# Kernel optimization log

Hardware: AMD Instinct MI355X
Metric: run time of the kernel (lower is better)

## Reference

```python
import jax, jax.numpy as jnp
import numpy as np

# Geometry constants matching __init__ defaults
DG = 2        # deformable_groups
KS = 3        # kernel_size
K = KS * KS   # taps per kernel
DIL = 2       # dilation
PAD = 2       # padding = dilation
STRIDE = 1


def setup_inputs() -> dict:
    key = jax.random.key(0)
    k1, k2, k3, k4 = jax.random.split(key, 4)
    B, C, H, W = 4, 128, 96, 192
    Cout = 128
    x = jax.random.normal(k1, (B, C, H, W), dtype=jnp.float32)
    # offset/mask conv: grouped conv, groups=DG -> in-channels per group = C//DG
    off_out = DG * 3 * K  # 54 (36 offset + 18 mask)
    # small weights so learned offsets are O(1) pixels (realistic trained regime;
    # the original zero-init would make the gather trivial)
    w_offset = jax.random.normal(k2, (off_out, C // DG, KS, KS), dtype=jnp.float32) * 0.01
    b_offset = jax.random.normal(k3, (off_out,), dtype=jnp.float32) * 0.1
    stdv = 1.0 / np.sqrt(C * KS * KS)
    w_deform = jax.random.uniform(k4, (Cout, C, KS, KS), dtype=jnp.float32,
                                  minval=-stdv, maxval=stdv)
    return {"x": x, "w_offset": w_offset, "b_offset": b_offset, "w_deform": w_deform}


def _deform_conv2d(x, w_offset, b_offset, w_deform):
    B, C, H, W = x.shape
    Cout = w_deform.shape[0]
    Cg = C // DG
    # --- offset/mask conv (grouped, dilated) ---
    om = jax.lax.conv_general_dilated(
        x, w_offset, (STRIDE, STRIDE), [(PAD, PAD), (PAD, PAD)],
        rhs_dilation=(DIL, DIL), feature_group_count=DG,
        dimension_numbers=("NCHW", "OIHW", "NCHW"))
    om = om + b_offset[None, :, None, None]
    Ho, Wo = om.shape[2], om.shape[3]
    off_ch = DG * 2 * K
    offset = om[:, :off_ch]                       # [B, 36, Ho, Wo]
    mask = jax.nn.sigmoid(om[:, off_ch:]) * 2.0   # double_mask=True -> *2
    # torchvision layout: channel 2*(g*K+k) = dy, +1 = dx
    off = offset.reshape(B, DG, K, 2, Ho, Wo)
    m = mask.reshape(B, DG, K, Ho, Wo)
    # --- sampling coordinates ---
    ky = (jnp.arange(K) // KS).astype(x.dtype)
    kx = (jnp.arange(K) % KS).astype(x.dtype)
    base_y = (jnp.arange(Ho) * STRIDE - PAD).astype(x.dtype)
    base_x = (jnp.arange(Wo) * STRIDE - PAD).astype(x.dtype)
    py = base_y[None, None, None, :, None] + (ky * DIL)[None, None, :, None, None] + off[:, :, :, 0]
    px = base_x[None, None, None, None, :] + (kx * DIL)[None, None, :, None, None] + off[:, :, :, 1]
    y0 = jnp.floor(py)
    x0 = jnp.floor(px)
    ty = py - y0
    tx = px - x0
    xflat = x.reshape(B, DG, Cg, H * W)
    # gather[b,g,c,n] = xflat[b,g,c, idx[b,g,n]]
    gather = jax.vmap(jax.vmap(lambda xg, idx: jnp.take(xg, idx, axis=1)))
    val = jnp.zeros((B, DG, Cg, K, Ho, Wo), x.dtype)
    # accumulate bilinear corners one at a time to bound peak memory
    for dy, dx, wgt in ((0, 0, (1 - ty) * (1 - tx)), (0, 1, (1 - ty) * tx),
                        (1, 0, ty * (1 - tx)), (1, 1, ty * tx)):
        yy = y0 + dy
        xx = x0 + dx
        valid = (yy >= 0) & (yy < H) & (xx >= 0) & (xx < W)
        yc = jnp.clip(yy, 0, H - 1).astype(jnp.int32)
        xc = jnp.clip(xx, 0, W - 1).astype(jnp.int32)
        lin = (yc * W + xc).reshape(B, DG, K * Ho * Wo)
        g = gather(xflat, lin).reshape(B, DG, Cg, K, Ho, Wo)
        val = val + jnp.where(valid, wgt, 0.0)[:, :, None] * g
    val = val * m[:, :, None]  # modulation mask per deformable group / tap
    wr = w_deform.reshape(Cout, DG, Cg, K)
    return jnp.einsum("ogck,bgckhw->bohw", wr, val)


def reference(x, w_offset, b_offset, w_deform):
    return _deform_conv2d(x, w_offset, b_offset, w_deform)
```

## Files before the change

### kernel.cpp

```cpp
#include <hip/hip_runtime.h>
#include <hip/hip_fp16.h>
#include <math.h>

#define BB   4
#define C_   128
#define H_   96
#define W_   192
#define COUT 128
#define DG_  2
#define CG_  64
#define K_   9
#define HO   96
#define WO   192
#define HW   (H_ * W_)
#define OMCH 54
#define RDIM (C_ * K_)
#define NKS  (RDIM / 32)
#define CSTEP 2
#define NCH  (NKS / CSTEP)
#define VROW 18

#define BARRIER() do {                                        \
    asm volatile("s_waitcnt lgkmcnt(0)" ::: "memory");        \
    __builtin_amdgcn_s_barrier();                             \
    asm volatile("" ::: "memory");                            \
  } while (0)

typedef __attribute__((ext_vector_type(8))) _Float16 f16x8;
typedef __attribute__((ext_vector_type(4))) float f32x4;

static __device__ __forceinline__ ushort f2bf(float f) {
  union { float f; uint u; } v; v.f = f;
  uint r = v.u + 0x7fff + ((v.u >> 16) & 1);
  return (ushort)(r >> 16);
}

__global__ __launch_bounds__(256) void prep_k(
    const float* __restrict__ wd, const float* __restrict__ wo,
    ushort* __restrict__ WtA, ushort* __restrict__ Awo2) {
  int i = blockIdx.x * 256 + threadIdx.x;
  if (i < 128 * RDIM) {
    int blkA = i >> 9, within = i & 511;
    int oct = within >> 7, colA = (within >> 3) & 15, j = within & 7;
    int m = blkA & 1, wvq = (blkA >> 1) & 3, s = blkA >> 3;
    int o = wvq * 32 + m * 16 + colA;
    int r = s * 32 + oct * 8 + j;
    int g = r / 576, t = r - g * 576;
    int k = t >> 6, cg = t & 63;
    WtA[i] = __half_as_ushort(__float2half(wd[((size_t)o * C_ + g * 64 + cg) * 9 + k]));
  }
  if (i < 64 * RDIM) {
    int blkA = i >> 9, within = i & 511;
    int oct = within >> 7, colA = (within >> 3) & 15, j = within & 7;
    int wv2 = blkA & 3, s = blkA >> 2;
    int o2 = wv2 * 16 + colA;
    int r = s * 32 + oct * 8 + j;
    int g = r / 576, t = r - g * 576;
    int k = t >> 6, cg = t & 63;
    int g2 = o2 >> 5, j2 = o2 & 31;
    float v = ((g2 == g) && (j2 < 27))
                ? wo[(((size_t)(g2 * 27 + j2)) * 64 + cg) * 9 + k] : 0.f;
    Awo2[i] = __half_as_ushort(__float2half(v));
  }
}

__global__ __launch_bounds__(256) void xt_k(
    const float* __restrict__ x, __half* __restrict__ xT) {
  __shared__ float t[128][65];
  int blk = blockIdx.x;
  int b = blk / 288, p0 = (blk % 288) * 64;
  int q = threadIdx.x >> 6, l = threadIdx.x & 63;
  const float* xb = x + (size_t)b * C_ * HW;
#pragma unroll
  for (int it = 0; it < 32; ++it) {
    int c = q * 32 + it;
    t[c][l] = xb[(size_t)c * HW + p0 + l];
  }
  __syncthreads();
  uint* xTb = (uint*)(xT + (size_t)b * HW * 128);
#pragma unroll
  for (int it = 0; it < 16; ++it) {
    int px = q * 16 + it;
    union { __half2 h; uint u; } pk;
    pk.h = __half2{__float2half(t[2 * l][px]), __float2half(t[2 * l + 1][px])};
    xTb[(size_t)(p0 + px) * 64 + l] = pk.u;
  }
}

__global__ __launch_bounds__(256, 5) void offset_nhwc_k(
    const __half* __restrict__ xT, const ushort* __restrict__ Awo2,
    const float* __restrict__ b_offset, float* __restrict__ om) {
  __shared__ uint s_val[3][CSTEP * 64 * VROW];

  int bid = blockIdx.x;
  int blk = (bid & 7) * 144 + (bid >> 3);
  int wt = blk % 3, bh = blk / 3;
  int ho = bh % HO, b = bh / HO;
  int wo0 = wt * 64;
  int tid = threadIdx.x;
  int lane = tid & 63, wv = tid >> 6;
  int sub = lane >> 3, q = lane & 7;
  int col = lane & 15, oct = lane >> 4;

  const __half* xTb = xT + (size_t)b * HW * 128;

  f32x4 acc[4];
#pragma unroll
  for (int n = 0; n < 4; ++n) acc[n] = (f32x4){0.f, 0.f, 0.f, 0.f};

  uint4 A0[2], B0[2];
  uint  MKa[2], MKb[2];
  int   IXa[2], IXb[2];

  auto issue = [&](int c, uint4 (&K0)[2], uint (&MK)[2], int (&IX)[2]) {
#pragma unroll
    for (int t = 0; t < 2; ++t) {
      int po = wv * 2 + t;
      int gk = c;
      int px = po * 8 + sub;
      int g = gk >= 9, k = gk - 9 * g;
      int dy = k / 3, dx = k - dy * 3;
      int y  = ho - 2 + 2 * dy;
      int xc = wo0 + px - 2 + 2 * dx;
      bool ok = (y >= 0) & (y < H_) & (xc >= 0) & (xc < W_);
      int yc  = min(max(y, 0), H_ - 1);
      int xcc = min(max(xc, 0), W_ - 1);
      const __half* p = xTb + (size_t)(yc * W_ + xcc) * 128 + g * 64 + q * 8;
      K0[t] = *(const uint4*)(p);
      MK[t] = ok ? 0x3c003c00u : 0u;
      IX[t] = ((q >> 2) * 64 + px) * VROW + (q & 3) * 4;
    }
  };

  auto finish = [&](int nb, const uint4 (&K0)[2], const uint (&MK)[2],
                    const int (&IX)[2]) {
#pragma unroll
    for (int t = 0; t < 2; ++t) {
      union { __half2 h2; uint u; } m; m.u = MK[t];
      uint res[4];
      const uint* a = (const uint*)&K0[t];
#pragma unroll
      for (int h = 0; h < 4; ++h) {
        union { __half2 h2; uint u; } p, vv;
        p.u = a[h];
        vv.h2 = __hmul2(p.h2, m.h2);
        res[h] = vv.u;
      }
      *(uint4*)&s_val[nb][IX[t]] = make_uint4(res[0], res[1], res[2], res[3]);
    }
  };

  auto loadA = [&](int c, f16x8 (&a0)[CSTEP]) {
#pragma unroll
    for (int ls = 0; ls < CSTEP; ++ls) {
      int s = c * CSTEP + ls;
      a0[ls] = *(const f16x8*)(Awo2 + (size_t)(s * 4 + wv) * 512 + (oct * 16 + col) * 8);
    }
  };

  auto compute = [&](int cb, const f16x8 (&a0)[CSTEP]) {
#pragma unroll
    for (int ls = 0; ls < CSTEP; ++ls) {
#pragma unroll
      for (int n = 0; n < 4; ++n) {
        f16x8 bfr = *(const f16x8*)
            &s_val[cb][(ls * 64 + n * 16 + col) * VROW + oct * 4];
        acc[n] = __builtin_amdgcn_mfma_f32_16x16x32_f16(a0[ls], bfr, acc[n], 0, 0, 0);
      }
    }
  };

  issue(0, A0, MKa, IXa);
  issue(1, B0, MKb, IXb);
  finish(0, A0, MKa, IXa);
  BARRIER();

  for (int c2 = 0; c2 < NCH; c2 += 2) {
    { int c = c2;
      f16x8 af[CSTEP];
      loadA(c, af);
      if (c + 2 < NCH) issue(c + 2, A0, MKa, IXa);
      compute(c % 3, af);
      finish((c + 1) % 3, B0, MKb, IXb);
      BARRIER();
    }
    { int c = c2 + 1;
      f16x8 af[CSTEP];
      loadA(c, af);
      if (c + 2 < NCH) issue(c + 2, B0, MKb, IXb);
      compute(c % 3, af);
      if (c + 1 < NCH) finish((c + 1) % 3, A0, MKa, IXa);
      BARRIER();
    }
  }

#pragma unroll
  for (int n = 0; n < 4; ++n)
#pragma unroll
    for (int ri = 0; ri < 4; ++ri) {
      int o2 = wv * 16 + oct * 4 + ri;
      int g = o2 >> 5, j = o2 & 31;
      if (j < 27) {
        int ch = g * 27 + j;
        om[((size_t)(b * OMCH + ch) * HO + ho) * WO + wo0 + n * 16 + col] =
            acc[n][ri] + b_offset[ch];
      }
    }
}

__global__ __launch_bounds__(256, 3) void deform_main_k(
    const __half* __restrict__ xT, const float* __restrict__ om,
    const ushort* __restrict__ WtA, float* __restrict__ out) {
  __shared__ uint  s_addr[18 * 64];
  __shared__ uint2 s_wq[18 * 64];
  __shared__ uint  s_val[3][CSTEP * 64 * VROW];

  int bid = blockIdx.x;
  int blk = (bid & 7) * 144 + (bid >> 3);
  int wt = blk % 3, bh = blk / 3;
  int ho = bh % HO, b = bh / HO;
  int wo0 = wt * 64;
  int tid = threadIdx.x;
  int lane = tid & 63, wv = tid >> 6;

  for (int e = tid; e < 18 * 64; e += 256) {
    int px = e & 63, gk = e >> 6;
    int g = gk / 9, k = gk - g * 9;
    int wo = wo0 + px;
    const float* omb = om + (size_t)b * OMCH * HW + (size_t)ho * WO + wo;
    float offy = omb[(size_t)(g * 18 + k * 2 + 0) * HW];
    float offx = omb[(size_t)(g * 18 + k * 2 + 1) * HW];
    float z    = omb[(size_t)(36 + g * 9 + k) * HW];
    float msk  = 2.f / (1.f + __expf(-z));
    float py = (float)(ho - 2 + (k / 3) * 2) + offy;
    float px_ = (float)(wo - 2 + (k % 3) * 2) + offx;
    float y0f = floorf(py), x0f = floorf(px_);
    int   y0 = (int)y0f, x0 = (int)x0f;
    float ty = py - y0f, tx = px_ - x0f;
    float wy0 = (y0 >= 0 && y0 < H_)      ? (1.f - ty) : 0.f;
    float wy1 = (y0 >= -1 && y0 < H_ - 1) ? ty         : 0.f;
    float wx0 = (x0 >= 0 && x0 < W_)      ? (1.f - tx) : 0.f;
    float wx1 = (x0 >= -1 && x0 < W_ - 1) ? tx         : 0.f;
    int yb  = min(max(y0, 0), H_ - 2);
    int xb_ = min(max(x0, 0), W_ - 2);
    float wAy = (y0 == yb      ? wy0 : 0.f) + (y0 + 1 == yb      ? wy1 : 0.f);
    float wBy = (y0 == yb + 1  ? wy0 : 0.f) + (y0 + 1 == yb + 1  ? wy1 : 0.f);
    float wAx = (x0 == xb_     ? wx0 : 0.f) + (x0 + 1 == xb_     ? wx1 : 0.f);
    float wBx = (x0 == xb_ + 1 ? wx0 : 0.f) + (x0 + 1 == xb_ + 1 ? wx1 : 0.f);
    s_addr[e] = (uint)((yb * W_ + xb_) * 128);
    union { __half2 h; uint u; } uA, uB;
    uA.h = __half2{__float2half(wAy * wAx * msk), __float2half(wAy * wBx * msk)};
    uB.h = __half2{__float2half(wBy * wAx * msk), __float2half(wBy * wBx * msk)};
    s_wq[e] = make_uint2(uA.u, uB.u);
  }

  const __half* xTb = xT + (size_t)b * HW * 128;
  int sub = lane >> 3, q = lane & 7;
  int col = lane & 15, oct = lane >> 4;

  f32x4 acc[2][4];
#pragma unroll
  for (int m = 0; m < 2; ++m)
#pragma unroll
    for (int n = 0; n < 4; ++n) acc[m][n] = (f32x4){0.f, 0.f, 0.f, 0.f};

  uint4 A0[2], A1[2], A2[2], A3[2];
  uint4 B0[2], B1[2], B2[2], B3[2];
  uint2 WQa[2], WQb[2];
  int   IXa[2], IXb[2];

  auto issue = [&](int c, uint4 (&K0)[2], uint4 (&K1)[2], uint4 (&K2)[2],
                   uint4 (&K3)[2], uint2 (&WQ)[2], int (&IX)[2]) {
#pragma unroll
    for (int t = 0; t < 2; ++t) {
      int po = wv * 2 + t;
      int gk = c;
      int px = po * 8 + sub;
      int ci = gk * 64 + px;
      uint base = s_addr[ci];
      WQ[t] = s_wq[ci];
      int g = gk >= 9;
      const __half* p = xTb + base + g * 64 + q * 8;
      K0[t] = *(const uint4*)(p);
      K1[t] = *(const uint4*)(p + 128);
      K2[t] = *(const uint4*)(p + W_ * 128);
      K3[t] = *(const uint4*)(p + W_ * 128 + 128);
      IX[t] = ((q >> 2) * 64 + px) * VROW + (q & 3) * 4;
    }
  };

  auto finish = [&](int nb, const uint4 (&K0)[2], const uint4 (&K1)[2],
                    const uint4 (&K2)[2], const uint4 (&K3)[2],
                    const uint2 (&WQ)[2], const int (&IX)[2]) {
#pragma unroll
    for (int t = 0; t < 2; ++t) {
      union { __half2 h; uint u; } w0, w1;
      w0.u = WQ[t].x; w1.u = WQ[t].y;
      __half2 wAx = __low2half2(w0.h), wAy = __high2half2(w0.h);
      __half2 wBx = __low2half2(w1.h), wBy = __high2half2(w1.h);
      uint res[4];
      const uint* a  = (const uint*)&K0[t];
      const uint* b1 = (const uint*)&K1[t];
      const uint* c2 = (const uint*)&K2[t];
      const uint* d  = (const uint*)&K3[t];
#pragma unroll
      for (int h = 0; h < 4; ++h) {
        union { __half2 h2; uint u; } p0, p1, p2, p3, vv;
        p0.u = a[h]; p1.u = b1[h]; p2.u = c2[h]; p3.u = d[h];
        __half2 v = __hmul2(p0.h2, wAx);
        v = __hfma2(p1.h2, wAy, v);
        v = __hfma2(p2.h2, wBx, v);
        v = __hfma2(p3.h2, wBy, v);
        vv.h2 = v;
        res[h] = vv.u;
      }
      *(uint4*)&s_val[nb][IX[t]] = make_uint4(res[0], res[1], res[2], res[3]);
    }
  };

  auto loadA = [&](int c, f16x8 (&a0)[CSTEP], f16x8 (&a1)[CSTEP]) {
#pragma unroll
    for (int ls = 0; ls < CSTEP; ++ls) {
      int s = c * CSTEP + ls;
      const ushort* ab = WtA + (size_t)((s * 4 + wv) * 2) * 512 + (oct * 16 + col) * 8;
      a0[ls] = *(const f16x8*)(ab);
      a1[ls] = *(const f16x8*)(ab + 512);
    }
  };

  auto compute = [&](int cb, const f16x8 (&a0)[CSTEP], const f16x8 (&a1)[CSTEP]) {
#pragma unroll
    for (int ls = 0; ls < CSTEP; ++ls) {
#pragma unroll
      for (int n = 0; n < 4; ++n) {
        f16x8 bfr = *(const f16x8*)
            &s_val[cb][(ls * 64 + n * 16 + col) * VROW + oct * 4];
        acc[0][n] = __builtin_amdgcn_mfma_f32_16x16x32_f16(a0[ls], bfr, acc[0][n], 0, 0, 0);
        acc[1][n] = __builtin_amdgcn_mfma_f32_16x16x32_f16(a1[ls], bfr, acc[1][n], 0, 0, 0);
      }
    }
  };

  BARRIER();
  issue(0, A0, A1, A2, A3, WQa, IXa);
  issue(1, B0, B1, B2, B3, WQb, IXb);
  finish(0, A0, A1, A2, A3, WQa, IXa);
  BARRIER();

  for (int c2 = 0; c2 < NCH; c2 += 2) {
    { int c = c2;
      f16x8 af0[CSTEP], af1[CSTEP];
      loadA(c, af0, af1);
      if (c + 2 < NCH) issue(c + 2, A0, A1, A2, A3, WQa, IXa);
      compute(c % 3, af0, af1);
      finish((c + 1) % 3, B0, B1, B2, B3, WQb, IXb);
      BARRIER();
    }
    { int c = c2 + 1;
      f16x8 af0[CSTEP], af1[CSTEP];
      loadA(c, af0, af1);
      if (c + 2 < NCH) issue(c + 2, B0, B1, B2, B3, WQb, IXb);
      compute(c % 3, af0, af1);
      if (c + 1 < NCH) finish((c + 1) % 3, A0, A1, A2, A3, WQa, IXa);
      BARRIER();
    }
  }

#pragma unroll
  for (int m = 0; m < 2; ++m)
#pragma unroll
    for (int n = 0; n < 4; ++n)
#pragma unroll
      for (int ri = 0; ri < 4; ++ri) {
        int o = wv * 32 + m * 16 + oct * 4 + ri;
        out[((size_t)(b * COUT + o) * HO + ho) * WO + wo0 + n * 16 + col] = acc[m][n][ri];
      }
}

extern "C" void kernel_launch(void* const* d_in, const int* in_sizes, int n_in,
                              void* d_out, int out_size, void* d_ws, size_t ws_size,
                              hipStream_t stream) {
  const float* x        = (const float*)d_in[0];
  const float* w_offset = (const float*)d_in[1];
  const float* b_offset = (const float*)d_in[2];
  const float* w_deform = (const float*)d_in[3];
  float* out = (float*)d_out;

  char* ws = (char*)d_ws;
  float*  om   = (float*)ws;
  ushort* WtA  = (ushort*)(ws + 15925248);
  ushort* Awo2 = (ushort*)(ws + 15925248 + 294912);
  __half* xT   = (__half*)(ws + 15925248 + 294912 + 147456);

  prep_k<<<576, 256, 0, stream>>>(w_deform, w_offset, WtA, Awo2);
  xt_k<<<1152, 256, 0, stream>>>(x, xT);
  offset_nhwc_k<<<1152, 256, 0, stream>>>(xT, Awo2, b_offset, om);
  deform_main_k<<<1152, 256, 0, stream>>>(xT, om, WtA, out);
}
```

Baseline: 94.60 us.

## Fuse offset conv into deformable main kernel via shared-memory offset tile

Merges the offset/mask convolution kernel into the deformable sampling kernel. Each block first computes its 54x64 offset/mask tile with MFMA, keeps it in LDS inside the reused staging buffer, then builds sampling weights and runs the main GEMM. This removes the global round trip of the om tensor and one kernel launch. In exchange the fused kernel runs at lower occupancy for the offset phase (3 blocks instead of 5) and the offset and main phases are serialized within each block.

```diff
diff --git a/kernel.cpp b/kernel.cpp
--- a/kernel.cpp
+++ b/kernel.cpp
@@ -19,6 +19,7 @@
 #define CSTEP 2
 #define NCH  (NKS / CSTEP)
 #define VROW 18
+#define CHUNKU (CSTEP * 64 * VROW)
 
 #define BARRIER() do {                                        \
     asm volatile("s_waitcnt lgkmcnt(0)" ::: "memory");        \
@@ -28,12 +29,6 @@
 
 typedef __attribute__((ext_vector_type(8))) _Float16 f16x8;
 typedef __attribute__((ext_vector_type(4))) float f32x4;
-
-static __device__ __forceinline__ ushort f2bf(float f) {
-  union { float f; uint u; } v; v.f = f;
-  uint r = v.u + 0x7fff + ((v.u >> 16) & 1);
-  return (ushort)(r >> 16);
-}
 
 __global__ __launch_bounds__(256) void prep_k(
     const float* __restrict__ wd, const float* __restrict__ wo,
@@ -87,10 +82,13 @@
   }
 }
 
-__global__ __launch_bounds__(256, 5) void offset_nhwc_k(
-    const __half* __restrict__ xT, const ushort* __restrict__ Awo2,
-    const float* __restrict__ b_offset, float* __restrict__ om) {
-  __shared__ uint s_val[3][CSTEP * 64 * VROW];
+__global__ __launch_bounds__(256, 3) void fused_k(
+    const __half* __restrict__ xT, const ushort* __restrict__ WtA,
+    const ushort* __restrict__ Awo2, const float* __restrict__ b_offset,
+    float* __restrict__ out) {
+  __shared__ uint  s_addr[18 * 64];
+  __shared__ uint2 s_wq[18 * 64];
+  __shared__ uint  s_buf[3 * CHUNKU];
 
   int bid = blockIdx.x;
   int blk = (bid & 7) * 144 + (bid >> 3);
@@ -103,134 +101,112 @@
   int col = lane & 15, oct = lane >> 4;
 
   const __half* xTb = xT + (size_t)b * HW * 128;
-
-  f32x4 acc[4];
-#pragma unroll
-  for (int n = 0; n < 4; ++n) acc[n] = (f32x4){0.f, 0.f, 0.f, 0.f};
-
-  uint4 A0[2], B0[2];
-  uint  MKa[2], MKb[2];
-  int   IXa[2], IXb[2];
-
-  auto issue = [&](int c, uint4 (&K0)[2], uint (&MK)[2], int (&IX)[2]) {
-#pragma unroll
-    for (int t = 0; t < 2; ++t) {
-      int po = wv * 2 + t;
-      int gk = c;
-      int px = po * 8 + sub;
-      int g = gk >= 9, k = gk - 9 * g;
-      int dy = k / 3, dx = k - dy * 3;
-      int y  = ho - 2 + 2 * dy;
-      int xc = wo0 + px - 2 + 2 * dx;
-      bool ok = (y >= 0) & (y < H_) & (xc >= 0) & (xc < W_);
-      int yc  = min(max(y, 0), H_ - 1);
-      int xcc = min(max(xc, 0), W_ - 1);
-      const __half* p = xTb + (size_t)(yc * W_ + xcc) * 128 + g * 64 + q * 8;
-      K0[t] = *(const uint4*)(p);
-      MK[t] = ok ? 0x3c003c00u : 0u;
-      IX[t] = ((q >> 2) * 64 + px) * VROW + (q & 3) * 4;
-    }
-  };
-
-  auto finish = [&](int nb, const uint4 (&K0)[2], const uint (&MK)[2],
-                    const int (&IX)[2]) {
-#pragma unroll
-    for (int t = 0; t < 2; ++t) {
-      union { __half2 h2; uint u; } m; m.u = MK[t];
-      uint res[4];
-      const uint* a = (const uint*)&K0[t];
-#pragma unroll
-      for (int h = 0; h < 4; ++h) {
-        union { __half2 h2; uint u; } p, vv;
-        p.u = a[h];
-        vv.h2 = __hmul2(p.h2, m.h2);
-        res[h] = vv.u;
-      }
-      *(uint4*)&s_val[nb][IX[t]] = make_uint4(res[0], res[1], res[2], res[3]);
-    }
-  };
-
-  auto loadA = [&](int c, f16x8 (&a0)[CSTEP]) {
-#pragma unroll
-    for (int ls = 0; ls < CSTEP; ++ls) {
-      int s = c * CSTEP + ls;
-      a0[ls] = *(const f16x8*)(Awo2 + (size_t)(s * 4 + wv) * 512 + (oct * 16 + col) * 8);
-    }
-  };
-
-  auto compute = [&](int cb, const f16x8 (&a0)[CSTEP]) {
-#pragma unroll
-    for (int ls = 0; ls < CSTEP; ++ls) {
-#pragma unroll
-      for (int n = 0; n < 4; ++n) {
-        f16x8 bfr = *(const f16x8*)
-            &s_val[cb][(ls * 64 + n * 16 + col) * VROW + oct * 4];
-        acc[n] = __builtin_amdgcn_mfma_f32_16x16x32_f16(a0[ls], bfr, acc[n], 0, 0, 0);
-      }
-    }
-  };
-
-  issue(0, A0, MKa, IXa);
-  issue(1, B0, MKb, IXb);
-  finish(0, A0, MKa, IXa);
-  BARRIER();
-
-  for (int c2 = 0; c2 < NCH; c2 += 2) {
-    { int c = c2;
-      f16x8 af[CSTEP];
-      loadA(c, af);
-      if (c + 2 < NCH) issue(c + 2, A0, MKa, IXa);
-      compute(c % 3, af);
-      finish((c + 1) % 3, B0, MKb, IXb);
-      BARRIER();
-    }
-    { int c = c2 + 1;
-      f16x8 af[CSTEP];
-      loadA(c, af);
-      if (c + 2 < NCH) issue(c + 2, B0, MKb, IXb);
-      compute(c % 3, af);
-      if (c + 1 < NCH) finish((c + 1) % 3, A0, MKa, IXa);
-      BARRIER();
-    }
-  }
-
-#pragma unroll
-  for (int n = 0; n < 4; ++n)
-#pragma unroll
-    for (int ri = 0; ri < 4; ++ri) {
-      int o2 = wv * 16 + oct * 4 + ri;
-      int g = o2 >> 5, j = o2 & 31;
-      if (j < 27) {
-        int ch = g * 27 + j;
-        om[((size_t)(b * OMCH + ch) * HO + ho) * WO + wo0 + n * 16 + col] =
-            acc[n][ri] + b_offset[ch];
-      }
-    }
-}
-
-__global__ __launch_bounds__(256, 3) void deform_main_k(
-    const __half* __restrict__ xT, const float* __restrict__ om,
-    const ushort* __restrict__ WtA, float* __restrict__ out) {
-  __shared__ uint  s_addr[18 * 64];
-  __shared__ uint2 s_wq[18 * 64];
-  __shared__ uint  s_val[3][CSTEP * 64 * VROW];
-
-  int bid = blockIdx.x;
-  int blk = (bid & 7) * 144 + (bid >> 3);
-  int wt = blk % 3, bh = blk / 3;
-  int ho = bh % HO, b = bh / HO;
-  int wo0 = wt * 64;
-  int tid = threadIdx.x;
-  int lane = tid & 63, wv = tid >> 6;
+  float* om_tile = (float*)s_buf;
+
+  {
+    f32x4 accO[4];
+#pragma unroll
+    for (int n = 0; n < 4; ++n) accO[n] = (f32x4){0.f, 0.f, 0.f, 0.f};
+
+    uint4 A0[2], B0[2];
+    uint  MKa[2], MKb[2];
+    int   IXa[2], IXb[2];
+
+    auto issueO = [&](int c, uint4 (&K0)[2], uint (&MK)[2], int (&IX)[2]) {
+#pragma unroll
+      for (int t = 0; t < 2; ++t) {
+        int po = wv * 2 + t;
+        int gk = c;
+        int px = po * 8 + sub;
+        int g = gk >= 9, k = gk - 9 * g;
+        int dy = k / 3, dx = k - dy * 3;
+        int y  = ho - 2 + 2 * dy;
+        int xc = wo0 + px - 2 + 2 * dx;
+        bool ok = (y >= 0) & (y < H_) & (xc >= 0) & (xc < W_);
+        int yc  = min(max(y, 0), H_ - 1);
+        int xcc = min(max(xc, 0), W_ - 1);
+        const __half* p = xTb + (size_t)(yc * W_ + xcc) * 128 + g * 64 + q * 8;
+        K0[t] = *(const uint4*)(p);
+        MK[t] = ok ? 0x3c003c00u : 0u;
+        IX[t] = ((q >> 2) * 64 + px) * VROW + (q & 3) * 4;
+      }
+    };
+
+    auto finishO = [&](int nb, const uint4 (&K0)[2], const uint (&MK)[2],
+                       const int (&IX)[2]) {
+      uint* sv = s_buf + nb * CHUNKU;
+#pragma unroll
+      for (int t = 0; t < 2; ++t) {
+        union { __half2 h2; uint u; } m; m.u = MK[t];
+        uint res[4];
+        const uint* a = (const uint*)&K0[t];
+#pragma unroll
+        for (int h = 0; h < 4; ++h) {
+          union { __half2 h2; uint u; } p, vv;
+          p.u = a[h];
+          vv.h2 = __hmul2(p.h2, m.h2);
+          res[h] = vv.u;
+        }
+        *(uint4*)&sv[IX[t]] = make_uint4(res[0], res[1], res[2], res[3]);
+      }
+    };
+
+    auto computeO = [&](int c, int cb) {
+      uint* sv = s_buf + cb * CHUNKU;
+#pragma unroll
+      for (int ls = 0; ls < CSTEP; ++ls) {
+        int s = c * CSTEP + ls;
+        f16x8 a0 = *(const f16x8*)(Awo2 + (size_t)(s * 4 + wv) * 512
+                                   + (oct * 16 + col) * 8);
+#pragma unroll
+        for (int n = 0; n < 4; ++n) {
+          f16x8 bfr = *(const f16x8*)&sv[(ls * 64 + n * 16 + col) * VROW + oct * 4];
+          accO[n] = __builtin_amdgcn_mfma_f32_16x16x32_f16(a0, bfr, accO[n], 0, 0, 0);
+        }
+      }
+    };
+
+    issueO(0, A0, MKa, IXa);
+    issueO(1, B0, MKb, IXb);
+    finishO(0, A0, MKa, IXa);
+    BARRIER();
+
+    for (int c2 = 0; c2 < NCH; c2 += 2) {
+      { int c = c2;
+        if (c + 2 < NCH) issueO(c + 2, A0, MKa, IXa);
+        computeO(c, c % 3);
+        finishO((c + 1) % 3, B0, MKb, IXb);
+        BARRIER();
+      }
+      { int c = c2 + 1;
+        if (c + 2 < NCH) issueO(c + 2, B0, MKb, IXb);
+        computeO(c, c % 3);
+        if (c + 1 < NCH) finishO((c + 1) % 3, A0, MKa, IXa);
+        BARRIER();
+      }
+    }
+
+#pragma unroll
+    for (int n = 0; n < 4; ++n)
+#pragma unroll
+      for (int ri = 0; ri < 4; ++ri) {
+        int o2 = wv * 16 + oct * 4 + ri;
+        int g = o2 >> 5, j = o2 & 31;
+        if (j < 27) {
+          int ch = g * 27 + j;
+          om_tile[ch * 64 + n * 16 + col] = accO[n][ri] + b_offset[ch];
+        }
+      }
+    BARRIER();
+  }
 
   for (int e = tid; e < 18 * 64; e += 256) {
     int px = e & 63, gk = e >> 6;
     int g = gk / 9, k = gk - g * 9;
     int wo = wo0 + px;
-    const float* omb = om + (size_t)b * OMCH * HW + (size_t)ho * WO + wo;
-    float offy = omb[(size_t)(g * 18 + k * 2 + 0) * HW];
-    float offx = omb[(size_t)(g * 18 + k * 2 + 1) * HW];
-    float z    = omb[(size_t)(36 + g * 9 + k) * HW];
+    float offy = om_tile[(g * 18 + k * 2 + 0) * 64 + px];
+    float offx = om_tile[(g * 18 + k * 2 + 1) * 64 + px];
+    float z    = om_tile[(36 + g * 9 + k) * 64 + px];
     float msk  = 2.f / (1.f + __expf(-z));
     float py = (float)(ho - 2 + (k / 3) * 2) + offy;
     float px_ = (float)(wo - 2 + (k % 3) * 2) + offx;
@@ -253,10 +229,7 @@
     uB.h = __half2{__float2half(wBy * wAx * msk), __float2half(wBy * wBx * msk)};
     s_wq[e] = make_uint2(uA.u, uB.u);
   }
-
-  const __half* xTb = xT + (size_t)b * HW * 128;
-  int sub = lane >> 3, q = lane & 7;
-  int col = lane & 15, oct = lane >> 4;
+  BARRIER();
 
   f32x4 acc[2][4];
 #pragma unroll
@@ -292,6 +265,7 @@
   auto finish = [&](int nb, const uint4 (&K0)[2], const uint4 (&K1)[2],
                     const uint4 (&K2)[2], const uint4 (&K3)[2],
                     const uint2 (&WQ)[2], const int (&IX)[2]) {
+    uint* sv = s_buf + nb * CHUNKU;
 #pragma unroll
     for (int t = 0; t < 2; ++t) {
       union { __half2 h; uint u; } w0, w1;
@@ -314,7 +288,7 @@
         vv.h2 = v;
         res[h] = vv.u;
       }
-      *(uint4*)&s_val[nb][IX[t]] = make_uint4(res[0], res[1], res[2], res[3]);
+      *(uint4*)&sv[IX[t]] = make_uint4(res[0], res[1], res[2], res[3]);
     }
   };
 
@@ -329,19 +303,18 @@
   };
 
   auto compute = [&](int cb, const f16x8 (&a0)[CSTEP], const f16x8 (&a1)[CSTEP]) {
+    uint* sv = s_buf + cb * CHUNKU;
 #pragma unroll
     for (int ls = 0; ls < CSTEP; ++ls) {
 #pragma unroll
       for (int n = 0; n < 4; ++n) {
-        f16x8 bfr = *(const f16x8*)
-            &s_val[cb][(ls * 64 + n * 16 + col) * VROW + oct * 4];
+        f16x8 bfr = *(const f16x8*)&sv[(ls * 64 + n * 16 + col) * VROW + oct * 4];
         acc[0][n] = __builtin_amdgcn_mfma_f32_16x16x32_f16(a0[ls], bfr, acc[0][n], 0, 0, 0);
         acc[1][n] = __builtin_amdgcn_mfma_f32_16x16x32_f16(a1[ls], bfr, acc[1][n], 0, 0, 0);
       }
     }
   };
 
-  BARRIER();
   issue(0, A0, A1, A2, A3, WQa, IXa);
   issue(1, B0, B1, B2, B3, WQb, IXb);
   finish(0, A0, A1, A2, A3, WQa, IXa);
@@ -387,13 +360,11 @@
   float* out = (float*)d_out;
 
   char* ws = (char*)d_ws;
-  float*  om   = (float*)ws;
-  ushort* WtA  = (ushort*)(ws + 15925248);
-  ushort* Awo2 = (ushort*)(ws + 15925248 + 294912);
-  __half* xT   = (__half*)(ws + 15925248 + 294912 + 147456);
+  ushort* WtA  = (ushort*)ws;
+  ushort* Awo2 = (ushort*)(ws + 294912);
+  __half* xT   = (__half*)(ws + 294912 + 147456);
 
   prep_k<<<576, 256, 0, stream>>>(w_deform, w_offset, WtA, Awo2);
   xt_k<<<1152, 256, 0, stream>>>(x, xT);
-  offset_nhwc_k<<<1152, 256, 0, stream>>>(xT, Awo2, b_offset, om);
-  deform_main_k<<<1152, 256, 0, stream>>>(xT, om, WtA, out);
+  fused_k<<<1152, 256, 0, stream>>>(xT, WtA, Awo2, b_offset, out);
 }
```

Measured after the change: 215.1 us. +127.4%, slower.
